# Kernel tuning notes

Measured on AMD Instinct MI355X. Metric: run time of the kernel, lower is better.

Reference implementation:

```python
import jax, jax.numpy as jnp
import numpy as np

N, E, U, R = 20000, 200000, 32, 64
NTYPES = 95
CUTOFF = 5.0
LN_EPS = 1e-5


def _init_linear(key, fan_in, fan_out, bias=True, dtype=jnp.float32):
    kw, kb = jax.random.split(key)
    bound = 1.0 / np.sqrt(fan_in)
    W = jax.random.uniform(kw, (fan_in, fan_out), dtype, -bound, bound)
    if not bias:
        return W
    b = jax.random.uniform(kb, (fan_out,), dtype, -bound, bound)
    return W, b


def setup_inputs() -> dict:
    key = jax.random.key(0)
    ks = jax.random.split(key, 20)
    f = jnp.float32
    Wd1, bd1 = _init_linear(ks[6], R, U)
    Wd2, bd2 = _init_linear(ks[7], R, U)
    Wd3, bd3 = _init_linear(ks[8], R, U)
    Wemb2, bemb2 = _init_linear(ks[9], 2 * U, U)
    Wemb3, bemb3 = _init_linear(ks[10], R, U)
    Ws1, bs1 = _init_linear(ks[11], U, 2 * U)
    Ws2, bs2 = _init_linear(ks[12], 2 * U, 3 * U)
    return {
        "node_type": jax.random.randint(ks[0], (N,), 0, NTYPES),
        "edge_attr": jax.random.normal(ks[1], (E, R), f),
        "bond_dist": jax.random.uniform(ks[2], (E,), f, 0.1, CUTOFF),
        "bond_vec": jax.random.normal(ks[3], (E, 3), f),
        "src": jax.random.randint(ks[4], (E,), 0, N),
        "dst": jax.random.randint(ks[5], (E,), 0, N),
        "emb_table": jax.random.normal(ks[13], (NTYPES, U), f),
        "Wd1": Wd1, "bd1": bd1, "Wd2": Wd2, "bd2": bd2, "Wd3": Wd3, "bd3": bd3,
        "Wemb2": Wemb2, "bemb2": bemb2, "Wemb3": Wemb3, "bemb3": bemb3,
        "Wt0": _init_linear(ks[14], U, U, bias=False),
        "Wt1": _init_linear(ks[15], U, U, bias=False),
        "Wt2": _init_linear(ks[16], U, U, bias=False),
        "Ws1": Ws1, "bs1": bs1, "Ws2": Ws2, "bs2": bs2,
        "ln_g": jnp.ones((U,), f), "ln_b": jnp.zeros((U,), f),
    }


def reference(node_type, edge_attr, bond_dist, bond_vec, src, dst,
              emb_table, Wd1, bd1, Wd2, bd2, Wd3, bd3,
              Wemb2, bemb2, Wemb3, bemb3, Wt0, Wt1, Wt2,
              Ws1, bs1, Ws2, bs2, ln_g, ln_b):
    act = jax.nn.silu
    dt = edge_attr.dtype
    Z = emb_table[node_type]                                        # [N,U]
    # cosine cutoff
    C = 0.5 * (jnp.cos(jnp.pi * bond_dist / CUTOFF) + 1.0) * (bond_dist <= CUTOFF).astype(dt)
    W1 = (edge_attr @ Wd1 + bd1) * C[:, None]                       # [E,U]
    W2 = (edge_attr @ Wd2 + bd2) * C[:, None]
    W3 = (edge_attr @ Wd3 + bd3) * C[:, None]
    v = bond_vec / jnp.linalg.norm(bond_vec, axis=1, keepdims=True)  # [E,3]
    eye = jnp.eye(3, dtype=dt)
    zero = jnp.zeros_like(v[:, 0])
    # vector_to_skewtensor
    A = jnp.stack([zero, -v[:, 2], v[:, 1],
                   v[:, 2], zero, -v[:, 0],
                   -v[:, 1], v[:, 0], zero], axis=1).reshape(-1, 3, 3)
    # vector_to_symtensor (outer product is already symmetric)
    t = v[:, :, None] * v[:, None, :]                               # [E,3,3]
    S = t - (jnp.trace(t, axis1=-2, axis2=-1) / 3.0)[:, None, None] * eye
    # edge message: Zij = emb2([v_src, v_dst])
    Zij = jnp.concatenate([Z[src], Z[dst]], axis=1) @ Wemb2 + bemb2  # [E,U]
    fI = Zij * W1  # Zij * new_radial_tensor weights, fused (same math)
    fA = Zij * W2
    fS = Zij * W3
    Iedge = fI[:, :, None, None] * eye                              # [E,U,3,3]
    Aedge = fA[:, :, None, None] * A[:, None, :, :]
    Sedge = fS[:, :, None, None] * S[:, None, :, :]
    seg = lambda x: jax.ops.segment_sum(x, dst, num_segments=N)
    Ie, Ae, Se = seg(Iedge), seg(Aedge), seg(Sedge)                 # [N,U,3,3]
    # tensor_norm + LayerNorm
    nrm = jnp.sum((Ie + Ae + Se) ** 2, axis=(-2, -1))               # [N,U]
    mu = jnp.mean(nrm, axis=-1, keepdims=True)
    var = jnp.mean((nrm - mu) ** 2, axis=-1, keepdims=True)
    nrm = (nrm - mu) / jnp.sqrt(var + LN_EPS) * ln_g + ln_b
    # per-channel linear mixing of tensor components
    Ie = jnp.einsum('nuij,uv->nvij', Ie, Wt0)
    Ae = jnp.einsum('nuij,uv->nvij', Ae, Wt1)
    Se = jnp.einsum('nuij,uv->nvij', Se, Wt2)
    nrm = act(nrm @ Ws1 + bs1)
    nrm = act(nrm @ Ws2 + bs2)                                      # [N,3U]
    nrm = nrm.reshape(nrm.shape[0], U, 3)
    X = (nrm[..., 0, None, None] * Ie
         + nrm[..., 1, None, None] * Ae
         + nrm[..., 2, None, None] * Se)                            # [N,U,3,3]
    edge_feat = edge_attr @ Wemb3 + bemb3                           # [E,U]
    return X, edge_feat
```

## Files before the change

kernel.cpp:

```cpp
#include <hip/hip_runtime.h>


#define NPB 8
#define EPW 8

__device__ inline void atomAddF(float* p, float v) {
#if defined(__HIP_PLATFORM_AMD__)
    unsafeAtomicAdd(p, v);
#else
    atomicAdd(p, v);
#endif
}

__global__ void ptype_kernel(const float* __restrict__ emb,
                             const float* __restrict__ We2,
                             const float* __restrict__ be2,
                             float* __restrict__ Pt1, float* __restrict__ Pt2) {
    const int c = threadIdx.x & 31;
    const int t = blockIdx.x * 8 + (threadIdx.x >> 5);
    if (t < 95) {
        float p1 = 0.f, p2 = 0.f;
        for (int k = 0; k < 32; ++k) {
            const float z = emb[t * 32 + k];
            p1 = fmaf(z, We2[k * 32 + c], p1);
            p2 = fmaf(z, We2[(32 + k) * 32 + c], p2);
        }
        Pt1[t * 32 + c] = p1 + be2[c];
        Pt2[t * 32 + c] = p2;
    }
}

__global__ void prep_zero(const int* __restrict__ nt,
                          const float* __restrict__ Pt1, const float* __restrict__ Pt2,
                          float* __restrict__ acc,
                          float* __restrict__ P1, float* __restrict__ P2, int N) {
    const int i = blockIdx.x * 256 + threadIdx.x;
    if (i < N * 320) acc[i] = 0.0f;
    if (i < N * 32) {
        const int n = i >> 5, c = i & 31;
        const int t = nt[n];
        P1[i] = Pt1[t * 32 + c];
        P2[i] = Pt2[t * 32 + c];
    }
}

__global__ __launch_bounds__(256) void edge_kernel(
    const float* __restrict__ edge_attr,
    const float* __restrict__ bond_dist,
    const float* __restrict__ bond_vec,
    const int*   __restrict__ src,
    const int*   __restrict__ dst,
    const float* __restrict__ Wd1, const float* __restrict__ bd1,
    const float* __restrict__ Wd2, const float* __restrict__ bd2,
    const float* __restrict__ Wd3, const float* __restrict__ bd3,
    const float* __restrict__ We3, const float* __restrict__ be3,
    const float* __restrict__ P1,
    const float* __restrict__ P2,
    float* __restrict__ acc,
    float* __restrict__ efeat,
    int E)
{
    __shared__ float sW[4][64][32];
    const int tid = threadIdx.x;
    for (int i = tid; i < 4 * 2048; i += 256) {
        const int m = i >> 11, r = i & 2047;
        const float* W = (m == 0) ? Wd1 : (m == 1) ? Wd2 : (m == 2) ? Wd3 : We3;
        sW[m][r >> 5][r & 31] = W[r];
    }
    __syncthreads();

    const int lane = tid & 63;
    const int c = lane & 31;
    const int h = lane >> 5;
    const float bd1r = bd1[c], bd2r = bd2[c], bd3r = bd3[c], be3r = be3[c];
    const float* wbase = &sW[0][h * 32][c];

    const int wid = __builtin_amdgcn_readfirstlane((blockIdx.x * 256 + tid) >> 6);
    const int nw = gridDim.x * 4;
    const int ngroups = (E + EPW - 1) / EPW;

    for (int g = wid; g < ngroups; g += nw) {
        const int base = g * EPW;

        float xr[EPW];
#pragma unroll
        for (int j = 0; j < EPW; ++j) {
            int e = base + j; if (e >= E) e = E - 1;
            xr[j] = edge_attr[(size_t)e * 64 + lane];
        }

        float A0[EPW], A1[EPW], A2[EPW], A3[EPW];
#pragma unroll
        for (int j = 0; j < EPW; ++j) { A0[j] = 0.f; A1[j] = 0.f; A2[j] = 0.f; A3[j] = 0.f; }

#pragma unroll 8
        for (int kk = 0; kk < 32; ++kk) {
            const float w0 = wbase[kk * 32];
            const float w1 = wbase[kk * 32 + 2048];
            const float w2 = wbase[kk * 32 + 4096];
            const float w3 = wbase[kk * 32 + 6144];
#pragma unroll
            for (int j = 0; j < EPW; ++j) {
                const float xb = __shfl(xr[j], kk, 32);
                A0[j] = fmaf(xb, w0, A0[j]);
                A1[j] = fmaf(xb, w1, A1[j]);
                A2[j] = fmaf(xb, w2, A2[j]);
                A3[j] = fmaf(xb, w3, A3[j]);
            }
        }

#pragma unroll
        for (int jj = 0; jj < 4; ++jj) {
            const float sd0 = h ? A0[jj] : A0[jj + 4];
            const float sd1 = h ? A1[jj] : A1[jj + 4];
            const float sd2 = h ? A2[jj] : A2[jj + 4];
            const float sd3 = h ? A3[jj] : A3[jj + 4];
            const float mn0 = h ? A0[jj + 4] : A0[jj];
            const float mn1 = h ? A1[jj + 4] : A1[jj];
            const float mn2 = h ? A2[jj + 4] : A2[jj];
            const float mn3 = h ? A3[jj + 4] : A3[jj];
            const float t0 = mn0 + __shfl_xor(sd0, 32);
            const float t1 = mn1 + __shfl_xor(sd1, 32);
            const float t2 = mn2 + __shfl_xor(sd2, 32);
            const float t3 = mn3 + __shfl_xor(sd3, 32);

            const int e = base + jj + 4 * h;
            const bool val = (e < E);
            const int ec = val ? e : (E - 1);

            const float d = bond_dist[ec];
            const float C = (d <= 5.0f) ? 0.5f * (cosf(3.14159265358979323846f * d / 5.0f) + 1.0f) : 0.0f;
            float v0 = bond_vec[3 * (size_t)ec + 0];
            float v1 = bond_vec[3 * (size_t)ec + 1];
            float v2 = bond_vec[3 * (size_t)ec + 2];
            const float inv = 1.0f / sqrtf(v0 * v0 + v1 * v1 + v2 * v2);
            v0 *= inv; v1 *= inv; v2 *= inv;
            const float tr3 = (v0 * v0 + v1 * v1 + v2 * v2) * (1.0f / 3.0f);
            const float y00 = v0 * v0 - tr3, y11 = v1 * v1 - tr3, y22 = v2 * v2 - tr3;
            const float y01 = v0 * v1, y02 = v0 * v2, y12 = v1 * v2;

            const int si = src[ec], di = dst[ec];
            const float az = P1[(size_t)si * 32 + c] + P2[(size_t)di * 32 + c];

            const float a1v = t0 + bd1r;
            const float a2v = t1 + bd2r;
            const float a3v = t2 + bd3r;
            const float a4v = t3 + be3r;
            const float w1v = a1v * C, w2v = a2v * C, w3v = a3v * C;
            const float fI = az * w1v, fA = az * w2v, fS = az * w3v;

            if (val) {
                efeat[(size_t)e * 32 + c] = a4v;
                float* ap = acc + (size_t)di * 320 + c;
                atomAddF(ap,       fI);
                atomAddF(ap + 32,  fA * v0);
                atomAddF(ap + 64,  fA * v1);
                atomAddF(ap + 96,  fA * v2);
                atomAddF(ap + 128, fS * y00);
                atomAddF(ap + 160, fS * y01);
                atomAddF(ap + 192, fS * y02);
                atomAddF(ap + 224, fS * y11);
                atomAddF(ap + 256, fS * y12);
                atomAddF(ap + 288, fS * y22);
            }
        }
    }
}

__global__ __launch_bounds__(256) void node_kernel(
    const float* __restrict__ acc,
    const float* __restrict__ Wt0, const float* __restrict__ Wt1, const float* __restrict__ Wt2,
    const float* __restrict__ Ws1, const float* __restrict__ bs1,
    const float* __restrict__ Ws2, const float* __restrict__ bs2,
    const float* __restrict__ lng, const float* __restrict__ lnb,
    float* __restrict__ xout,
    int N, int ngroups)
{
    __shared__ float wtS[32][96];
    __shared__ float ws1[32][64];
    __shared__ float ws2[64][96];
    __shared__ float sb1[64], sb2[96], sg[32], sbv[32];
    __shared__ float4 accS4[NPB][32][3];
    __shared__ float nrmS[NPB][32];
    __shared__ float h1S[NPB][64];

    const int tid = threadIdx.x;
    for (int i = tid; i < 1024; i += 256) {
        const int k = i >> 5, u = i & 31;
        wtS[k][u]      = Wt0[i];
        wtS[k][32 + u] = Wt1[i];
        wtS[k][64 + u] = Wt2[i];
    }
    for (int i = tid; i < 2048; i += 256) ws1[i >> 6][i & 63] = Ws1[i];
    for (int i = tid; i < 6144; i += 256) ws2[i / 96][i % 96] = Ws2[i];
    if (tid < 64) sb1[tid] = bs1[tid];
    if (tid < 96) sb2[tid] = bs2[tid];
    if (tid < 32) { sg[tid] = lng[tid]; sbv[tid] = lnb[tid]; }
    __syncthreads();

    const int ln_ = tid >> 5, u = tid & 31;

    for (int g = blockIdx.x; g < ngroups; g += gridDim.x) {
        const int n = g * NPB + ln_;
        const bool valid = n < N;

        float c0 = 0, a0 = 0, a1 = 0, a2 = 0, s00 = 0, s01 = 0, s02 = 0, s11 = 0, s12 = 0, s22 = 0;
        if (valid) {
            const float* ap = acc + (size_t)n * 320 + u;
            c0 = ap[0];  a0 = ap[32];  a1 = ap[64];  a2 = ap[96];
            s00 = ap[128]; s01 = ap[160]; s02 = ap[192];
            s11 = ap[224]; s12 = ap[256]; s22 = ap[288];
        }
        accS4[ln_][u][0] = make_float4(c0, a0, a1, a2);
        accS4[ln_][u][1] = make_float4(s00, s01, s02, s11);
        accS4[ln_][u][2] = make_float4(s12, s22, 0.f, 0.f);

        const float m00 = c0 + s00, m11 = c0 + s11, m22 = c0 + s22;
        float nrm = m00 * m00 + m11 * m11 + m22 * m22
                  + 2.0f * (s01 * s01 + a2 * a2 + s02 * s02 + a1 * a1 + s12 * s12 + a0 * a0);

        float sum = nrm;
#pragma unroll
        for (int o = 16; o >= 1; o >>= 1) sum += __shfl_xor(sum, o, 32);
        const float mu = sum * (1.0f / 32.0f);
        const float dv = nrm - mu;
        float vs = dv * dv;
#pragma unroll
        for (int o = 16; o >= 1; o >>= 1) vs += __shfl_xor(vs, o, 32);
        const float var = vs * (1.0f / 32.0f);
        const float nl = dv * rsqrtf(var + 1e-5f) * sg[u] + sbv[u];
        nrmS[ln_][u] = nl;
        __syncthreads();

        float h1a = sb1[u], h1b = sb1[u + 32];
#pragma unroll
        for (int k = 0; k < 32; ++k) {
            const float x = nrmS[ln_][k];
            h1a += x * ws1[k][u];
            h1b += x * ws1[k][u + 32];
        }
        h1a = h1a / (1.0f + __expf(-h1a));
        h1b = h1b / (1.0f + __expf(-h1b));
        h1S[ln_][u] = h1a; h1S[ln_][u + 32] = h1b;
        __syncthreads();

        float f0 = sb2[3 * u], f1 = sb2[3 * u + 1], f2 = sb2[3 * u + 2];
#pragma unroll
        for (int k = 0; k < 64; ++k) {
            const float hh = h1S[ln_][k];
            f0 += hh * ws2[k][3 * u];
            f1 += hh * ws2[k][3 * u + 1];
            f2 += hh * ws2[k][3 * u + 2];
        }
        f0 = f0 / (1.0f + __expf(-f0));
        f1 = f1 / (1.0f + __expf(-f1));
        f2 = f2 / (1.0f + __expf(-f2));

        float m0 = 0, ma0 = 0, ma1 = 0, ma2 = 0;
        float ms00 = 0, ms01 = 0, ms02 = 0, ms11 = 0, ms12 = 0, ms22 = 0;
#pragma unroll
        for (int k = 0; k < 32; ++k) {
            const float w0 = wtS[k][u], w1 = wtS[k][32 + u], w2 = wtS[k][64 + u];
            const float4 q0 = accS4[ln_][k][0];
            const float4 q1 = accS4[ln_][k][1];
            const float4 q2 = accS4[ln_][k][2];
            m0   += q0.x * w0;
            ma0  += q0.y * w1;
            ma1  += q0.z * w1;
            ma2  += q0.w * w1;
            ms00 += q1.x * w2;
            ms01 += q1.y * w2;
            ms02 += q1.z * w2;
            ms11 += q1.w * w2;
            ms12 += q2.x * w2;
            ms22 += q2.y * w2;
        }
        if (valid) {
            float* xp = xout + (size_t)n * 288 + u * 9;
            xp[0] = f0 * m0 + f2 * ms00;
            xp[1] = f1 * (-ma2) + f2 * ms01;
            xp[2] = f1 * ( ma1) + f2 * ms02;
            xp[3] = f1 * ( ma2) + f2 * ms01;
            xp[4] = f0 * m0 + f2 * ms11;
            xp[5] = f1 * (-ma0) + f2 * ms12;
            xp[6] = f1 * (-ma1) + f2 * ms02;
            xp[7] = f1 * ( ma0) + f2 * ms12;
            xp[8] = f0 * m0 + f2 * ms22;
        }
        __syncthreads();
    }
}

extern "C" void kernel_launch(void* const* d_in, const int* in_sizes, int n_in,
                              void* d_out, int out_size, void* d_ws, size_t ws_size,
                              hipStream_t stream) {
    const int N = in_sizes[0];
    const int E = in_sizes[2];

    float* acc = (float*)d_ws;
    float* P1  = acc + (size_t)N * 320;
    float* P2  = P1 + (size_t)N * 32;
    float* Pt1 = P2 + (size_t)N * 32;
    float* Pt2 = Pt1 + 95 * 32;

    float* xout  = (float*)d_out;
    float* efeat = xout + (size_t)N * 288;

    ptype_kernel<<<12, 256, 0, stream>>>(
        (const float*)d_in[6], (const float*)d_in[13], (const float*)d_in[14], Pt1, Pt2);

    prep_zero<<<(N * 320 + 255) / 256, 256, 0, stream>>>(
        (const int*)d_in[0], Pt1, Pt2, acc, P1, P2, N);

    edge_kernel<<<1280, 256, 0, stream>>>(
        (const float*)d_in[1], (const float*)d_in[2], (const float*)d_in[3],
        (const int*)d_in[4], (const int*)d_in[5],
        (const float*)d_in[7],  (const float*)d_in[8],
        (const float*)d_in[9],  (const float*)d_in[10],
        (const float*)d_in[11], (const float*)d_in[12],
        (const float*)d_in[15], (const float*)d_in[16],
        P1, P2, acc, efeat, E);

    const int ngroups = (N + NPB - 1) / NPB;
    node_kernel<<<512, 256, 0, stream>>>(
        acc,
        (const float*)d_in[17], (const float*)d_in[18], (const float*)d_in[19],
        (const float*)d_in[20], (const float*)d_in[21],
        (const float*)d_in[22], (const float*)d_in[23],
        (const float*)d_in[24], (const float*)d_in[25],
        xout, N, ngroups);
}
```

Measured before the change: 430.8 us.

## Keep edge weights in registers, stage edge features in LDS, sync-free node kernel

The edge kernel now holds each lane's 128 weight values in registers instead of LDS, and stages the edge_attr rows for each wave through per-wave shared memory as float4. The inner product then reads vectorized LDS values instead of doing per-k shuffles. Per-edge scalars and the P1/P2 gathers are loaded earlier so their latency overlaps with the math. The node kernel packs its weights into float2/float4 LDS layouts, replaces LDS broadcast plus __syncthreads with sub-wave shuffles, drops per-iteration barriers, and cuts the edge grid to 768 blocks. The large register footprint risks lower occupancy or spills.

After: 429.1 us. Within noise of the previous version (-0.4%).

```diff
diff --git a/kernel.cpp b/kernel.cpp
--- a/kernel.cpp
+++ b/kernel.cpp
@@ -1,7 +1,6 @@
 #include <hip/hip_runtime.h>
 
 
-#define NPB 8
 #define EPW 8
 
 __device__ inline void atomAddF(float* p, float v) {
@@ -60,54 +59,88 @@
     float* __restrict__ efeat,
     int E)
 {
-    __shared__ float sW[4][64][32];
-    const int tid = threadIdx.x;
-    for (int i = tid; i < 4 * 2048; i += 256) {
-        const int m = i >> 11, r = i & 2047;
-        const float* W = (m == 0) ? Wd1 : (m == 1) ? Wd2 : (m == 2) ? Wd3 : We3;
-        sW[m][r >> 5][r & 31] = W[r];
-    }
-    __syncthreads();
-
+    __shared__ float4 sX[4][8][16];
+
+    const int tid  = threadIdx.x;
     const int lane = tid & 63;
-    const int c = lane & 31;
-    const int h = lane >> 5;
+    const int c    = lane & 31;
+    const int h    = lane >> 5;
+    const int wv   = tid >> 6;
+
+    float w0r[32], w1r[32], w2r[32], w3r[32];
+#pragma unroll
+    for (int kk = 0; kk < 32; ++kk) {
+        const int row = (h << 5) + kk;
+        w0r[kk] = Wd1[row * 32 + c];
+        w1r[kk] = Wd2[row * 32 + c];
+        w2r[kk] = Wd3[row * 32 + c];
+        w3r[kk] = We3[row * 32 + c];
+    }
     const float bd1r = bd1[c], bd2r = bd2[c], bd3r = bd3[c], be3r = be3[c];
-    const float* wbase = &sW[0][h * 32][c];
-
-    const int wid = __builtin_amdgcn_readfirstlane((blockIdx.x * 256 + tid) >> 6);
-    const int nw = gridDim.x * 4;
+
+    float4 (*sXw)[16] = sX[wv];
+
+    const int wid = (blockIdx.x * 256 + tid) >> 6;
+    const int nw  = gridDim.x * 4;
     const int ngroups = (E + EPW - 1) / EPW;
 
     for (int g = wid; g < ngroups; g += nw) {
         const int base = g * EPW;
 
-        float xr[EPW];
-#pragma unroll
-        for (int j = 0; j < EPW; ++j) {
-            int e = base + j; if (e >= E) e = E - 1;
-            xr[j] = edge_attr[(size_t)e * 64 + lane];
+        int si4[4], di4[4];
+        float dd[4], vx[4], vy[4], vz[4];
+#pragma unroll
+        for (int jj = 0; jj < 4; ++jj) {
+            int e = base + jj + (h << 2); if (e >= E) e = E - 1;
+            si4[jj] = src[e]; di4[jj] = dst[e];
+            dd[jj]  = bond_dist[e];
+            vx[jj]  = bond_vec[3 * (size_t)e + 0];
+            vy[jj]  = bond_vec[3 * (size_t)e + 1];
+            vz[jj]  = bond_vec[3 * (size_t)e + 2];
+        }
+
+        {
+            int ea = base + (lane >> 4);     if (ea >= E) ea = E - 1;
+            int eb = base + 4 + (lane >> 4); if (eb >= E) eb = E - 1;
+            const float4 xa = *(const float4*)&edge_attr[(size_t)ea * 64 + (lane & 15) * 4];
+            const float4 xb = *(const float4*)&edge_attr[(size_t)eb * 64 + (lane & 15) * 4];
+            sXw[lane >> 4][lane & 15]     = xa;
+            sXw[4 + (lane >> 4)][lane & 15] = xb;
         }
 
         float A0[EPW], A1[EPW], A2[EPW], A3[EPW];
 #pragma unroll
         for (int j = 0; j < EPW; ++j) { A0[j] = 0.f; A1[j] = 0.f; A2[j] = 0.f; A3[j] = 0.f; }
 
-#pragma unroll 8
-        for (int kk = 0; kk < 32; ++kk) {
-            const float w0 = wbase[kk * 32];
-            const float w1 = wbase[kk * 32 + 2048];
-            const float w2 = wbase[kk * 32 + 4096];
-            const float w3 = wbase[kk * 32 + 6144];
+#pragma unroll
+        for (int kq = 0; kq < 8; ++kq) {
+            const int k0 = kq * 4;
 #pragma unroll
             for (int j = 0; j < EPW; ++j) {
-                const float xb = __shfl(xr[j], kk, 32);
-                A0[j] = fmaf(xb, w0, A0[j]);
-                A1[j] = fmaf(xb, w1, A1[j]);
-                A2[j] = fmaf(xb, w2, A2[j]);
-                A3[j] = fmaf(xb, w3, A3[j]);
+                const float4 xq = sXw[j][(h << 3) + kq];
+                A0[j] = fmaf(xq.x, w0r[k0 + 0], A0[j]);
+                A0[j] = fmaf(xq.y, w0r[k0 + 1], A0[j]);
+                A0[j] = fmaf(xq.z, w0r[k0 + 2], A0[j]);
+                A0[j] = fmaf(xq.w, w0r[k0 + 3], A0[j]);
+                A1[j] = fmaf(xq.x, w1r[k0 + 0], A1[j]);
+                A1[j] = fmaf(xq.y, w1r[k0 + 1], A1[j]);
+                A1[j] = fmaf(xq.z, w1r[k0 + 2], A1[j]);
+                A1[j] = fmaf(xq.w, w1r[k0 + 3], A1[j]);
+                A2[j] = fmaf(xq.x, w2r[k0 + 0], A2[j]);
+                A2[j] = fmaf(xq.y, w2r[k0 + 1], A2[j]);
+                A2[j] = fmaf(xq.z, w2r[k0 + 2], A2[j]);
+                A2[j] = fmaf(xq.w, w2r[k0 + 3], A2[j]);
+                A3[j] = fmaf(xq.x, w3r[k0 + 0], A3[j]);
+                A3[j] = fmaf(xq.y, w3r[k0 + 1], A3[j]);
+                A3[j] = fmaf(xq.z, w3r[k0 + 2], A3[j]);
+                A3[j] = fmaf(xq.w, w3r[k0 + 3], A3[j]);
             }
         }
+
+        float az4[4];
+#pragma unroll
+        for (int jj = 0; jj < 4; ++jj)
+            az4[jj] = P1[(size_t)si4[jj] * 32 + c] + P2[(size_t)di4[jj] * 32 + c];
 
 #pragma unroll
         for (int jj = 0; jj < 4; ++jj) {
@@ -126,22 +159,17 @@
 
             const int e = base + jj + 4 * h;
             const bool val = (e < E);
-            const int ec = val ? e : (E - 1);
-
-            const float d = bond_dist[ec];
+
+            const float d = dd[jj];
             const float C = (d <= 5.0f) ? 0.5f * (cosf(3.14159265358979323846f * d / 5.0f) + 1.0f) : 0.0f;
-            float v0 = bond_vec[3 * (size_t)ec + 0];
-            float v1 = bond_vec[3 * (size_t)ec + 1];
-            float v2 = bond_vec[3 * (size_t)ec + 2];
+            float v0 = vx[jj], v1 = vy[jj], v2 = vz[jj];
             const float inv = 1.0f / sqrtf(v0 * v0 + v1 * v1 + v2 * v2);
             v0 *= inv; v1 *= inv; v2 *= inv;
             const float tr3 = (v0 * v0 + v1 * v1 + v2 * v2) * (1.0f / 3.0f);
             const float y00 = v0 * v0 - tr3, y11 = v1 * v1 - tr3, y22 = v2 * v2 - tr3;
             const float y01 = v0 * v1, y02 = v0 * v2, y12 = v1 * v2;
 
-            const int si = src[ec], di = dst[ec];
-            const float az = P1[(size_t)si * 32 + c] + P2[(size_t)di * 32 + c];
-
+            const float az = az4[jj];
             const float a1v = t0 + bd1r;
             const float a2v = t1 + bd2r;
             const float a3v = t2 + bd3r;
@@ -151,7 +179,7 @@
 
             if (val) {
                 efeat[(size_t)e * 32 + c] = a4v;
-                float* ap = acc + (size_t)di * 320 + c;
+                float* ap = acc + (size_t)di4[jj] * 320 + c;
                 atomAddF(ap,       fI);
                 atomAddF(ap + 32,  fA * v0);
                 atomAddF(ap + 64,  fA * v1);
@@ -174,46 +202,46 @@
     const float* __restrict__ Ws2, const float* __restrict__ bs2,
     const float* __restrict__ lng, const float* __restrict__ lnb,
     float* __restrict__ xout,
-    int N, int ngroups)
+    int N)
 {
-    __shared__ float wtS[32][96];
-    __shared__ float ws1[32][64];
-    __shared__ float ws2[64][96];
-    __shared__ float sb1[64], sb2[96], sg[32], sbv[32];
-    __shared__ float4 accS4[NPB][32][3];
-    __shared__ float nrmS[NPB][32];
-    __shared__ float h1S[NPB][64];
+    __shared__ float4 wtp[32][32];
+    __shared__ float2 ws1p[32][32];
+    __shared__ float4 ws2p[64][32];
+    __shared__ float4 accS4[8][32][3];
+    __shared__ float2 sb1p[32];
+    __shared__ float4 sb2p[32];
+    __shared__ float  sg[32], sbv[32];
 
     const int tid = threadIdx.x;
     for (int i = tid; i < 1024; i += 256) {
         const int k = i >> 5, u = i & 31;
-        wtS[k][u]      = Wt0[i];
-        wtS[k][32 + u] = Wt1[i];
-        wtS[k][64 + u] = Wt2[i];
-    }
-    for (int i = tid; i < 2048; i += 256) ws1[i >> 6][i & 63] = Ws1[i];
-    for (int i = tid; i < 6144; i += 256) ws2[i / 96][i % 96] = Ws2[i];
-    if (tid < 64) sb1[tid] = bs1[tid];
-    if (tid < 96) sb2[tid] = bs2[tid];
-    if (tid < 32) { sg[tid] = lng[tid]; sbv[tid] = lnb[tid]; }
+        wtp[k][u]  = make_float4(Wt0[i], Wt1[i], Wt2[i], 0.f);
+        ws1p[k][u] = make_float2(Ws1[k * 64 + u], Ws1[k * 64 + 32 + u]);
+    }
+    for (int i = tid; i < 2048; i += 256) {
+        const int k = i >> 5, u = i & 31;
+        ws2p[k][u] = make_float4(Ws2[k * 96 + 3 * u], Ws2[k * 96 + 3 * u + 1],
+                                 Ws2[k * 96 + 3 * u + 2], 0.f);
+    }
+    if (tid < 32) {
+        sb1p[tid] = make_float2(bs1[tid], bs1[tid + 32]);
+        sb2p[tid] = make_float4(bs2[3 * tid], bs2[3 * tid + 1], bs2[3 * tid + 2], 0.f);
+        sg[tid] = lng[tid]; sbv[tid] = lnb[tid];
+    }
     __syncthreads();
 
-    const int ln_ = tid >> 5, u = tid & 31;
-
-    for (int g = blockIdx.x; g < ngroups; g += gridDim.x) {
-        const int n = g * NPB + ln_;
-        const bool valid = n < N;
-
-        float c0 = 0, a0 = 0, a1 = 0, a2 = 0, s00 = 0, s01 = 0, s02 = 0, s11 = 0, s12 = 0, s22 = 0;
-        if (valid) {
-            const float* ap = acc + (size_t)n * 320 + u;
-            c0 = ap[0];  a0 = ap[32];  a1 = ap[64];  a2 = ap[96];
-            s00 = ap[128]; s01 = ap[160]; s02 = ap[192];
-            s11 = ap[224]; s12 = ap[256]; s22 = ap[288];
-        }
-        accS4[ln_][u][0] = make_float4(c0, a0, a1, a2);
-        accS4[ln_][u][1] = make_float4(s00, s01, s02, s11);
-        accS4[ln_][u][2] = make_float4(s12, s22, 0.f, 0.f);
+    const int hw = tid >> 5, u = tid & 31;
+    const int stride = gridDim.x * 8;
+
+    for (int n = blockIdx.x * 8 + hw; n < N; n += stride) {
+        const float* ap = acc + (size_t)n * 320 + u;
+        const float c0 = ap[0],   a0 = ap[32],  a1 = ap[64],  a2 = ap[96];
+        const float s00 = ap[128], s01 = ap[160], s02 = ap[192];
+        const float s11 = ap[224], s12 = ap[256], s22 = ap[288];
+
+        accS4[hw][u][0] = make_float4(c0, a0, a1, a2);
+        accS4[hw][u][1] = make_float4(s00, s01, s02, s11);
+        accS4[hw][u][2] = make_float4(s12, s22, 0.f, 0.f);
 
         const float m00 = c0 + s00, m11 = c0 + s11, m22 = c0 + s22;
         float nrm = m00 * m00 + m11 * m11 + m22 * m22
@@ -229,28 +257,36 @@
         for (int o = 16; o >= 1; o >>= 1) vs += __shfl_xor(vs, o, 32);
         const float var = vs * (1.0f / 32.0f);
         const float nl = dv * rsqrtf(var + 1e-5f) * sg[u] + sbv[u];
-        nrmS[ln_][u] = nl;
-        __syncthreads();
-
-        float h1a = sb1[u], h1b = sb1[u + 32];
-#pragma unroll
-        for (int k = 0; k < 32; ++k) {
-            const float x = nrmS[ln_][k];
-            h1a += x * ws1[k][u];
-            h1b += x * ws1[k][u + 32];
+
+        const float2 b1 = sb1p[u];
+        float h1a = b1.x, h1b = b1.y;
+#pragma unroll
+        for (int k = 0; k < 32; ++k) {
+            const float x = __shfl(nl, k, 32);
+            const float2 wq = ws1p[k][u];
+            h1a = fmaf(x, wq.x, h1a);
+            h1b = fmaf(x, wq.y, h1b);
         }
         h1a = h1a / (1.0f + __expf(-h1a));
         h1b = h1b / (1.0f + __expf(-h1b));
-        h1S[ln_][u] = h1a; h1S[ln_][u + 32] = h1b;
-        __syncthreads();
-
-        float f0 = sb2[3 * u], f1 = sb2[3 * u + 1], f2 = sb2[3 * u + 2];
-#pragma unroll
-        for (int k = 0; k < 64; ++k) {
-            const float hh = h1S[ln_][k];
-            f0 += hh * ws2[k][3 * u];
-            f1 += hh * ws2[k][3 * u + 1];
-            f2 += hh * ws2[k][3 * u + 2];
+
+        const float4 b2 = sb2p[u];
+        float f0 = b2.x, f1 = b2.y, f2 = b2.z;
+#pragma unroll
+        for (int k = 0; k < 32; ++k) {
+            const float hh = __shfl(h1a, k, 32);
+            const float4 wq = ws2p[k][u];
+            f0 = fmaf(hh, wq.x, f0);
+            f1 = fmaf(hh, wq.y, f1);
+            f2 = fmaf(hh, wq.z, f2);
+        }
+#pragma unroll
+        for (int k = 0; k < 32; ++k) {
+            const float hh = __shfl(h1b, k, 32);
+            const float4 wq = ws2p[32 + k][u];
+            f0 = fmaf(hh, wq.x, f0);
+            f1 = fmaf(hh, wq.y, f1);
+            f2 = fmaf(hh, wq.z, f2);
         }
         f0 = f0 / (1.0f + __expf(-f0));
         f1 = f1 / (1.0f + __expf(-f1));
@@ -260,34 +296,32 @@
         float ms00 = 0, ms01 = 0, ms02 = 0, ms11 = 0, ms12 = 0, ms22 = 0;
 #pragma unroll
         for (int k = 0; k < 32; ++k) {
-            const float w0 = wtS[k][u], w1 = wtS[k][32 + u], w2 = wtS[k][64 + u];
-            const float4 q0 = accS4[ln_][k][0];
-            const float4 q1 = accS4[ln_][k][1];
-            const float4 q2 = accS4[ln_][k][2];
-            m0   += q0.x * w0;
-            ma0  += q0.y * w1;
-            ma1  += q0.z * w1;
-            ma2  += q0.w * w1;
-            ms00 += q1.x * w2;
-            ms01 += q1.y * w2;
-            ms02 += q1.z * w2;
-            ms11 += q1.w * w2;
-            ms12 += q2.x * w2;
-            ms22 += q2.y * w2;
-        }
-        if (valid) {
-            float* xp = xout + (size_t)n * 288 + u * 9;
-            xp[0] = f0 * m0 + f2 * ms00;
-            xp[1] = f1 * (-ma2) + f2 * ms01;
-            xp[2] = f1 * ( ma1) + f2 * ms02;
-            xp[3] = f1 * ( ma2) + f2 * ms01;
-            xp[4] = f0 * m0 + f2 * ms11;
-            xp[5] = f1 * (-ma0) + f2 * ms12;
-            xp[6] = f1 * (-ma1) + f2 * ms02;
-            xp[7] = f1 * ( ma0) + f2 * ms12;
-            xp[8] = f0 * m0 + f2 * ms22;
-        }
-        __syncthreads();
+            const float4 w  = wtp[k][u];
+            const float4 q0 = accS4[hw][k][0];
+            const float4 q1 = accS4[hw][k][1];
+            const float4 q2 = accS4[hw][k][2];
+            m0   = fmaf(q0.x, w.x, m0);
+            ma0  = fmaf(q0.y, w.y, ma0);
+            ma1  = fmaf(q0.z, w.y, ma1);
+            ma2  = fmaf(q0.w, w.y, ma2);
+            ms00 = fmaf(q1.x, w.z, ms00);
+            ms01 = fmaf(q1.y, w.z, ms01);
+            ms02 = fmaf(q1.z, w.z, ms02);
+            ms11 = fmaf(q1.w, w.z, ms11);
+            ms12 = fmaf(q2.x, w.z, ms12);
+            ms22 = fmaf(q2.y, w.z, ms22);
+        }
+
+        float* xp = xout + (size_t)n * 288 + u * 9;
+        xp[0] = f0 * m0 + f2 * ms00;
+        xp[1] = f1 * (-ma2) + f2 * ms01;
+        xp[2] = f1 * ( ma1) + f2 * ms02;
+        xp[3] = f1 * ( ma2) + f2 * ms01;
+        xp[4] = f0 * m0 + f2 * ms11;
+        xp[5] = f1 * (-ma0) + f2 * ms12;
+        xp[6] = f1 * (-ma1) + f2 * ms02;
+        xp[7] = f1 * ( ma0) + f2 * ms12;
+        xp[8] = f0 * m0 + f2 * ms22;
     }
 }
 
@@ -312,7 +346,7 @@
     prep_zero<<<(N * 320 + 255) / 256, 256, 0, stream>>>(
         (const int*)d_in[0], Pt1, Pt2, acc, P1, P2, N);
 
-    edge_kernel<<<1280, 256, 0, stream>>>(
+    edge_kernel<<<768, 256, 0, stream>>>(
         (const float*)d_in[1], (const float*)d_in[2], (const float*)d_in[3],
         (const int*)d_in[4], (const int*)d_in[5],
         (const float*)d_in[7],  (const float*)d_in[8],
@@ -321,12 +355,11 @@
         (const float*)d_in[15], (const float*)d_in[16],
         P1, P2, acc, efeat, E);
 
-    const int ngroups = (N + NPB - 1) / NPB;
     node_kernel<<<512, 256, 0, stream>>>(
         acc,
         (const float*)d_in[17], (const float*)d_in[18], (const float*)d_in[19],
         (const float*)d_in[20], (const float*)d_in[21],
         (const float*)d_in[22], (const float*)d_in[23],
         (const float*)d_in[24], (const float*)d_in[25],
-        xout, N, ngroups);
-}
+        xout, N);
+}
```
